# Performance work log

Measured on AMD Instinct MI355X. Metric: run time of the kernel, lower is better.

The kernel has to match this reference:

```python
import jax, jax.numpy as jnp
import numpy as np

N_NODES = 50000


def _graph_conv(x, edges, W0, b0, W1, b1):
    # Symmetric (undirected) message passing: each edge (a,b) sends x[b]->a and x[a]->b.
    src = jnp.concatenate([edges[:, 0], edges[:, 1]])  # [2E]
    dst = jnp.concatenate([edges[:, 1], edges[:, 0]])  # [2E]
    deg = jax.ops.segment_sum(jnp.ones_like(dst, dtype=x.dtype), dst, num_segments=N_NODES)
    deg = jnp.maximum(deg, 1.0)  # avoid div-by-zero for isolated nodes
    agg = jax.ops.segment_sum(x[src], dst, num_segments=N_NODES) / deg[:, None]  # [N, F]
    # self transform + normalized-neighbor transform
    return x @ W0 + b0 + agg @ W1 + b1


def setup_inputs() -> dict:
    key = jax.random.key(0)
    ks = jax.random.split(key, 10)
    feats = [256, 512, 256]  # [in] + hidden + [out]
    inp = {
        "vert_features": jax.random.normal(ks[0], (N_NODES, feats[0]), dtype=jnp.float32),
        "edges": jax.random.randint(ks[1], (400000, 2), 0, N_NODES, dtype=jnp.int64),
    }
    kidx = 2
    for l, (fi, fo) in enumerate(zip(feats[:-1], feats[1:])):
        s = 1.0 / np.sqrt(fi)
        inp[f"W0_{l}"] = jax.random.normal(ks[kidx], (fi, fo), dtype=jnp.float32) * s
        inp[f"b0_{l}"] = jnp.zeros((fo,), dtype=jnp.float32)
        inp[f"W1_{l}"] = jax.random.normal(ks[kidx + 1], (fi, fo), dtype=jnp.float32) * s
        inp[f"b1_{l}"] = jnp.zeros((fo,), dtype=jnp.float32)
        kidx += 2
    return inp


def reference(vert_features, edges, W0_0, b0_0, W1_0, b1_0, W0_1, b0_1, W1_1, b1_1):
    # layer 0 + ReLU
    x = _graph_conv(vert_features, edges, W0_0, b0_0, W1_0, b1_0)
    x = jax.nn.relu(x)
    # final layer (no activation)
    x = _graph_conv(x, edges, W0_1, b0_1, W1_1, b1_1)
    return x
```

## Files before the change

kernel.cpp:

```cpp
#include <hip/hip_runtime.h>
#include <stdint.h>

typedef __bf16  bf16x8 __attribute__((ext_vector_type(8)));
typedef float   f32x4  __attribute__((ext_vector_type(4)));
typedef unsigned short u16x8 __attribute__((ext_vector_type(8)));

__device__ __forceinline__ unsigned short f2bf(float f) {
  unsigned int u = __float_as_uint(f);
  u += 0x7fffu + ((u >> 16) & 1u);
  return (unsigned short)(u >> 16);
}
__device__ __forceinline__ float bflo(unsigned int v) { return __uint_as_float(v << 16); }
__device__ __forceinline__ float bfhi(unsigned int v) { return __uint_as_float(v & 0xffff0000u); }

__device__ __forceinline__ int edges_are_i64(const int* __restrict__ eg) {
  return (eg[1] | eg[3] | eg[5] | eg[7]) == 0;
}

__global__ void phase1_kernel(const float* __restrict__ x, unsigned short* __restrict__ A0, int n,
                              const int* __restrict__ eg, int* __restrict__ deg, int E,
                              const float* __restrict__ W00, const float* __restrict__ W10,
                              const float* __restrict__ W01, const float* __restrict__ W11,
                              const float* __restrict__ b00, const float* __restrict__ b10,
                              const float* __restrict__ b01, const float* __restrict__ b11,
                              unsigned short* __restrict__ Bt1, unsigned short* __restrict__ Bt2,
                              float* __restrict__ bias1, float* __restrict__ bias2) {
  const int i = blockIdx.x * 256 + threadIdx.x;
  if (i < n * 64) {
    const int row = i >> 6, c4 = i & 63;
    const float4 v = ((const float4*)x)[i];
    ushort4 o;
    o.x = f2bf(v.x); o.y = f2bf(v.y); o.z = f2bf(v.z); o.w = f2bf(v.w);
    *(ushort4*)&A0[(size_t)row * 512 + c4 * 4] = o;
  }
  if (i < 512 * 512) {
    const int nn = i >> 9, k = i & 511;
    const float v1 = (k < 256) ? W00[k * 512 + nn] : W10[(k - 256) * 512 + nn];
    Bt1[i] = f2bf(v1);
    const float v2 = (nn < 256) ? W01[k * 256 + nn] : W11[k * 256 + (nn - 256)];
    Bt2[i] = f2bf(v2);
    if (i < 512) {
      bias1[i] = b00[i] + b10[i];
      bias2[i] = (i < 256) ? (b01[i] + b11[i]) : 0.f;
    }
  }
  if (i < E) {
    int a, b;
    if (edges_are_i64(eg)) { a = eg[4 * i]; b = eg[4 * i + 2]; }
    else                   { a = eg[2 * i]; b = eg[2 * i + 1]; }
    if ((unsigned)a < (unsigned)n && (unsigned)b < (unsigned)n) {
      atomicAdd(&deg[a], 1);
      atomicAdd(&deg[b], 1);
    }
  }
}

__global__ void block_sum_kernel(const int* __restrict__ deg, int* __restrict__ bsum, int n) {
  const int t = threadIdx.x;
  const int i = blockIdx.x * 1024 + t;
  int v = (i < n) ? deg[i] : 0;
  #pragma unroll
  for (int d = 32; d > 0; d >>= 1) v += __shfl_xor(v, d);
  __shared__ int ws[16];
  if ((t & 63) == 0) ws[t >> 6] = v;
  __syncthreads();
  if (t < 16) {
    int s = ws[t];
    #pragma unroll
    for (int d = 1; d < 16; d <<= 1) s += __shfl_xor(s, d);
    if (t == 0) bsum[blockIdx.x] = s;
  }
}

__global__ void scan_bsum_kernel(int* __restrict__ bsum, int* __restrict__ off, int nb, int n) {
  const int l = threadIdx.x;
  int v = (l < nb) ? bsum[l] : 0;
  const int orig = v;
  #pragma unroll
  for (int d = 1; d < 64; d <<= 1) {
    int u = __shfl_up(v, d);
    if (l >= d) v += u;
  }
  if (l < nb) bsum[l] = v - orig;
  if (l == nb - 1) off[n] = v;
}

__global__ void scan_final_kernel(const int* __restrict__ deg, const int* __restrict__ bsum,
                                  int* __restrict__ off, float* __restrict__ invd,
                                  int* __restrict__ curp, int n) {
  const int t = threadIdx.x;
  const int i = blockIdx.x * 1024 + t;
  const int lane = t & 63, wid = t >> 6;
  const int v = (i < n) ? deg[i] : 0;
  int s = v;
  #pragma unroll
  for (int d = 1; d < 64; d <<= 1) {
    int u = __shfl_up(s, d);
    if (lane >= d) s += u;
  }
  __shared__ int ws[16];
  if (lane == 63) ws[wid] = s;
  __syncthreads();
  if (t < 16) {
    int w = ws[t];
    #pragma unroll
    for (int d = 1; d < 16; d <<= 1) {
      int u = __shfl_up(w, d);
      if (t >= d) w += u;
    }
    ws[t] = w;
  }
  __syncthreads();
  const int add = (wid > 0) ? ws[wid - 1] : 0;
  const int incl = s + add;
  if (i < n) {
    off[i] = bsum[blockIdx.x] + incl - v;
    invd[i] = 1.f / (float)(v > 1 ? v : 1);
    curp[i] = 0;
  }
}

__global__ void fill_kernel(const int* __restrict__ eg,
                            const int* __restrict__ off, int* __restrict__ cur,
                            int* __restrict__ adj, int E, int n) {
  const int e = blockIdx.x * 256 + threadIdx.x;
  if (e >= E) return;
  int a, b;
  if (edges_are_i64(eg)) { a = eg[4 * e]; b = eg[4 * e + 2]; }
  else                   { a = eg[2 * e]; b = eg[2 * e + 1]; }
  if ((unsigned)a >= (unsigned)n || (unsigned)b >= (unsigned)n) return;
  int p = atomicAdd(&cur[b], 1); adj[off[b] + p] = a;
  int q = atomicAdd(&cur[a], 1); adj[off[a] + q] = b;
}

template<int MODE>
__global__ __launch_bounds__(256) void agg_wide_kernel(
    const unsigned short* __restrict__ T, unsigned short* A0w, float* out,
    const int* __restrict__ adj, const int* __restrict__ off,
    const float* __restrict__ invd, int n) {
  const int node = blockIdx.x * 4 + (threadIdx.x >> 6);
  if (node >= n) return;
  const int lane = threadIdx.x & 63;
  const int half = lane >> 5;
  const int cq = lane & 31;
  constexpr size_t RS = (MODE == 0) ? 512 : 256;
  const int s = off[node], e = off[node + 1];
  float a0 = 0.f, a1 = 0.f, a2 = 0.f, a3 = 0.f, a4 = 0.f, a5 = 0.f, a6 = 0.f, a7 = 0.f;
  for (int base = s; base < e; base += 64) {
    const int cnt = min(64, e - base);
    const int idxv = (lane < cnt) ? adj[base + lane] : 0;
    for (int j = 0; j < cnt; j += 8) {
      uint4 v0 = make_uint4(0u, 0u, 0u, 0u), v1 = v0, v2 = v0, v3 = v0;
      const int s0 = j + 0 + half, s1 = j + 2 + half, s2 = j + 4 + half, s3 = j + 6 + half;
      const int r0 = __shfl(idxv, s0), r1 = __shfl(idxv, s1);
      const int r2 = __shfl(idxv, s2), r3 = __shfl(idxv, s3);
      if (s0 < cnt) v0 = *(const uint4*)&T[(size_t)r0 * RS + cq * 8];
      if (s1 < cnt) v1 = *(const uint4*)&T[(size_t)r1 * RS + cq * 8];
      if (s2 < cnt) v2 = *(const uint4*)&T[(size_t)r2 * RS + cq * 8];
      if (s3 < cnt) v3 = *(const uint4*)&T[(size_t)r3 * RS + cq * 8];
      a0 += bflo(v0.x) + bflo(v1.x) + bflo(v2.x) + bflo(v3.x);
      a1 += bfhi(v0.x) + bfhi(v1.x) + bfhi(v2.x) + bfhi(v3.x);
      a2 += bflo(v0.y) + bflo(v1.y) + bflo(v2.y) + bflo(v3.y);
      a3 += bfhi(v0.y) + bfhi(v1.y) + bfhi(v2.y) + bfhi(v3.y);
      a4 += bflo(v0.z) + bflo(v1.z) + bflo(v2.z) + bflo(v3.z);
      a5 += bfhi(v0.z) + bfhi(v1.z) + bfhi(v2.z) + bfhi(v3.z);
      a6 += bflo(v0.w) + bflo(v1.w) + bflo(v2.w) + bflo(v3.w);
      a7 += bfhi(v0.w) + bfhi(v1.w) + bfhi(v2.w) + bfhi(v3.w);
    }
  }
  a0 += __shfl_xor(a0, 32); a1 += __shfl_xor(a1, 32);
  a2 += __shfl_xor(a2, 32); a3 += __shfl_xor(a3, 32);
  a4 += __shfl_xor(a4, 32); a5 += __shfl_xor(a5, 32);
  a6 += __shfl_xor(a6, 32); a7 += __shfl_xor(a7, 32);
  if (half == 0) {
    const float sc = invd[node];
    if (MODE == 0) {
      u16x8 o;
      o[0] = f2bf(a0 * sc); o[1] = f2bf(a1 * sc); o[2] = f2bf(a2 * sc); o[3] = f2bf(a3 * sc);
      o[4] = f2bf(a4 * sc); o[5] = f2bf(a5 * sc); o[6] = f2bf(a6 * sc); o[7] = f2bf(a7 * sc);
      *(u16x8*)&A0w[(size_t)node * 512 + 256 + cq * 8] = o;
    } else {
      float* po = &out[(size_t)node * 256 + cq * 8];
      float4 p0 = *(float4*)po;
      float4 p1 = *(float4*)(po + 4);
      p0.x += sc * a0; p0.y += sc * a1; p0.z += sc * a2; p0.w += sc * a3;
      p1.x += sc * a4; p1.y += sc * a5; p1.z += sc * a6; p1.w += sc * a7;
      *(float4*)po = p0;
      *(float4*)(po + 4) = p1;
    }
  }
}

template<int MODE>
__global__ __launch_bounds__(256, 2) void gemm_kernel(
    const unsigned short* __restrict__ A, const unsigned short* __restrict__ Bt,
    const float* __restrict__ bias,
    unsigned short* __restrict__ Hout, float* __restrict__ Pout, unsigned short* __restrict__ Zout,
    int M_real, int nwg) {
  constexpr int K = 512;
  constexpr int BK = 64;
  constexpr int NT = K / BK;
  __shared__ unsigned short sm[4][128 * BK];
  const int t = threadIdx.x;
  const int lane = t & 63;
  const int wid = t >> 6;
  const int wr = wid >> 1;
  const int wc = wid & 1;

  const int orig = blockIdx.x;
  const int q = nwg >> 3, r = nwg & 7;
  const int xcd = orig & 7, bidx = orig >> 3;
  const int wgid = (xcd < r ? xcd * (q + 1) : r * (q + 1) + (xcd - r) * q) + bidx;
  const int m0 = (wgid >> 2) * 128;
  const int n0 = (wgid & 3) * 128;

  f32x4 acc[4][4];
  #pragma unroll
  for (int m = 0; m < 4; ++m)
    #pragma unroll
    for (int n = 0; n < 4; ++n)
      acc[m][n] = f32x4{0.f, 0.f, 0.f, 0.f};

  const int srow = t >> 3;
  const int schunk = t & 7;

  auto stage = [&](int buf, int kt) {
    #pragma unroll
    for (int i = 0; i < 4; ++i) {
      const int row = srow + i * 32;
      const int c = schunk ^ (row & 7);
      const unsigned short* ga = A + (size_t)(m0 + row) * K + kt * BK + c * 8;
      __builtin_amdgcn_global_load_lds(
          (const __attribute__((address_space(1))) unsigned int*)ga,
          (__attribute__((address_space(3))) unsigned int*)&sm[buf][(i * 256 + t) * 8], 16, 0, 0);
    }
    #pragma unroll
    for (int i = 0; i < 4; ++i) {
      const int row = srow + i * 32;
      const int c = schunk ^ (row & 7);
      const unsigned short* gb = Bt + (size_t)(n0 + row) * K + kt * BK + c * 8;
      __builtin_amdgcn_global_load_lds(
          (const __attribute__((address_space(1))) unsigned int*)gb,
          (__attribute__((address_space(3))) unsigned int*)&sm[2 + buf][(i * 256 + t) * 8], 16, 0, 0);
    }
    asm volatile("" ::: "memory");
    __builtin_amdgcn_sched_barrier(0);
  };

  auto compute = [&](int buf) {
    #pragma unroll
    for (int kk = 0; kk < 2; ++kk) {
      bf16x8 aF[4], bF[4];
      #pragma unroll
      for (int m = 0; m < 4; ++m) {
        const int row = wr * 64 + m * 16 + (lane & 15);
        const int sl = (kk * 4 + (lane >> 4)) ^ (row & 7);
        aF[m] = *(const bf16x8*)&sm[buf][row * BK + sl * 8];
      }
      #pragma unroll
      for (int n = 0; n < 4; ++n) {
        const int row = wc * 64 + n * 16 + (lane & 15);
        const int sl = (kk * 4 + (lane >> 4)) ^ (row & 7);
        bF[n] = *(const bf16x8*)&sm[2 + buf][row * BK + sl * 8];
      }
      #pragma unroll
      for (int m = 0; m < 4; ++m)
        #pragma unroll
        for (int n = 0; n < 4; ++n)
          acc[m][n] = __builtin_amdgcn_mfma_f32_16x16x32_bf16(aF[m], bF[n], acc[m][n], 0, 0, 0);
    }
  };

  stage(0, 0);
  #pragma unroll 1
  for (int kt = 0; kt < NT; ++kt) {
    if (kt + 1 < NT) stage((kt + 1) & 1, kt + 1);
    if (kt + 1 < NT) { asm volatile("s_waitcnt vmcnt(8)" ::: "memory"); }
    else             { asm volatile("s_waitcnt vmcnt(0)" ::: "memory"); }
    __builtin_amdgcn_sched_barrier(0);
    __builtin_amdgcn_s_barrier();
    __builtin_amdgcn_sched_barrier(0);
    compute(kt & 1);
    asm volatile("s_waitcnt lgkmcnt(0)" ::: "memory");
    __builtin_amdgcn_sched_barrier(0);
    __builtin_amdgcn_s_barrier();
    __builtin_amdgcn_sched_barrier(0);
  }
  __syncthreads();

  if (MODE == 0 || n0 >= 256) {
    unsigned short* ep = &sm[0][0];
    #pragma unroll
    for (int n = 0; n < 4; ++n) {
      const int lcol = wc * 64 + n * 16 + (lane & 15);
      const float bc = (MODE == 0) ? bias[n0 + lcol] : 0.f;
      #pragma unroll
      for (int m = 0; m < 4; ++m) {
        #pragma unroll
        for (int rr = 0; rr < 4; ++rr) {
          const int lr = wr * 64 + m * 16 + (lane >> 4) * 4 + rr;
          float y = acc[m][n][rr] + bc;
          if (MODE == 0) y = y > 0.f ? y : 0.f;
          ep[lr * 128 + (lcol ^ (((lr >> 2) & 7) << 4))] = f2bf(y);
        }
      }
    }
    __syncthreads();
    unsigned short* dst = (MODE == 0) ? Hout : Zout;
    const int ld = (MODE == 0) ? 512 : 256;
    const int cb0 = (MODE == 0) ? n0 : (n0 - 256);
    #pragma unroll
    for (int p = 0; p < 8; ++p) {
      const int tr = p * 16 + (t >> 4);
      const int cb = (t & 15) * 8;
      const uint4 v = *(const uint4*)&ep[tr * 128 + (cb ^ (((tr >> 2) & 7) << 4))];
      *(uint4*)&dst[(size_t)(m0 + tr) * ld + cb0 + cb] = v;
    }
  } else {
    float* ep = (float*)&sm[0][0];
    #pragma unroll
    for (int pp = 0; pp < 2; ++pp) {
      if (wr == pp) {
        #pragma unroll
        for (int n = 0; n < 4; ++n) {
          const int lcol = wc * 64 + n * 16 + (lane & 15);
          const float bc = bias[n0 + lcol];
          #pragma unroll
          for (int m = 0; m < 4; ++m)
            #pragma unroll
            for (int rr = 0; rr < 4; ++rr) {
              const int lr = m * 16 + (lane >> 4) * 4 + rr;
              ep[lr * 128 + (lcol ^ (((lr >> 2) & 7) << 4))] = acc[m][n][rr] + bc;
            }
        }
      }
      __syncthreads();
      const int tr = t >> 2;
      const int grow = m0 + pp * 64 + tr;
      if (grow < M_real) {
        #pragma unroll
        for (int j = 0; j < 8; ++j) {
          const int cb = (t & 3) * 32 + j * 4;
          const float4 v = *(const float4*)&ep[tr * 128 + (cb ^ (((tr >> 2) & 7) << 4))];
          *(float4*)&Pout[(size_t)grow * 256 + n0 + cb] = v;
        }
      }
      __syncthreads();
    }
  }
}

extern "C" void kernel_launch(void* const* d_in, const int* in_sizes, int n_in,
                              void* d_out, int out_size, void* d_ws, size_t ws_size,
                              hipStream_t stream) {
  const float* x   = (const float*)d_in[0];
  const int* edges = (const int*)d_in[1];
  const float* W00 = (const float*)d_in[2];
  const float* b00 = (const float*)d_in[3];
  const float* W10 = (const float*)d_in[4];
  const float* b10 = (const float*)d_in[5];
  const float* W01 = (const float*)d_in[6];
  const float* b01 = (const float*)d_in[7];
  const float* W11 = (const float*)d_in[8];
  const float* b11 = (const float*)d_in[9];
  float* out = (float*)d_out;

  const int n = in_sizes[0] / 256;
  const int E = in_sizes[1] / 2;
  const int Mpad = ((n + 127) / 128) * 128;

  char* p = (char*)d_ws;
  auto alloc = [&](size_t bytes) { char* r = p; p += (bytes + 255) & ~(size_t)255; return r; };
  unsigned short* A0   = (unsigned short*)alloc((size_t)Mpad * 512 * 2);
  unsigned short* H    = (unsigned short*)alloc((size_t)Mpad * 512 * 2);
  unsigned short* Z    = (unsigned short*)alloc((size_t)Mpad * 256 * 2);
  unsigned short* Bt1  = (unsigned short*)alloc(512 * 512 * 2);
  unsigned short* Bt2  = (unsigned short*)alloc(512 * 512 * 2);
  float* bias1 = (float*)alloc(512 * 4);
  float* bias2 = (float*)alloc(512 * 4);
  int*   deg   = (int*)alloc((size_t)n * 4);
  int*   curp  = (int*)alloc((size_t)n * 4);
  int*   off   = (int*)alloc((size_t)(n + 1) * 4);
  int*   bsum  = (int*)alloc(256 * 4);
  float* invd  = (float*)alloc((size_t)n * 4);
  int*   adj   = (int*)alloc((size_t)2 * E * 4);

  hipMemsetAsync(deg, 0, (size_t)n * 4, stream);

  const int p1_blocks = (n * 64 + 255) / 256;
  phase1_kernel<<<p1_blocks, 256, 0, stream>>>(x, A0, n, edges, deg, E,
                                               W00, W10, W01, W11, b00, b10, b01, b11,
                                               Bt1, Bt2, bias1, bias2);

  const int nb = (n + 1023) / 1024;
  block_sum_kernel<<<nb, 1024, 0, stream>>>(deg, bsum, n);
  scan_bsum_kernel<<<1, 64, 0, stream>>>(bsum, off, nb, n);
  scan_final_kernel<<<nb, 1024, 0, stream>>>(deg, bsum, off, invd, curp, n);
  fill_kernel<<<(E + 255) / 256, 256, 0, stream>>>(edges, off, curp, adj, E, n);

  agg_wide_kernel<0><<<(n + 3) / 4, 256, 0, stream>>>(A0, A0, nullptr, adj, off, invd, n);

  const int nwg = (Mpad / 128) * 4;
  gemm_kernel<0><<<nwg, 256, 0, stream>>>(A0, Bt1, bias1, H, nullptr, nullptr, n, nwg);
  gemm_kernel<1><<<nwg, 256, 0, stream>>>(H, Bt2, bias2, nullptr, out, Z, n, nwg);

  agg_wide_kernel<1><<<(n + 3) / 4, 256, 0, stream>>>(Z, nullptr, out, adj, off, invd, n);
}
```

Measured before the change: 321.1 us.

## Enlarge GEMM tile to 256x128 with 512-thread blocks and simpler barriers

The bf16 MFMA GEMM now uses 256x128 output tiles computed by 8 waves per block, where it used 128x128 tiles with 4 waves. Shared memory is split into separate A and B double buffers, row padding moves to 256, and the epilogues are adjusted to the taller tile. The aim is to load each B tile once for twice as many rows and to cut the number of workgroups. The hand-tuned vmcnt/lgkmcnt waits and sched barriers are replaced by plain __syncthreads, which may expose more of the load latency and drops the 2-blocks-per-CU occupancy hint.

After: 356.2 us. 1.11x slower.

```diff
diff --git a/kernel.cpp b/kernel.cpp
--- a/kernel.cpp
+++ b/kernel.cpp
@@ -192,7 +192,7 @@
 }
 
 template<int MODE>
-__global__ __launch_bounds__(256, 2) void gemm_kernel(
+__global__ __launch_bounds__(512, 1) void gemm_kernel(
     const unsigned short* __restrict__ A, const unsigned short* __restrict__ Bt,
     const float* __restrict__ bias,
     unsigned short* __restrict__ Hout, float* __restrict__ Pout, unsigned short* __restrict__ Zout,
@@ -200,7 +200,8 @@
   constexpr int K = 512;
   constexpr int BK = 64;
   constexpr int NT = K / BK;
-  __shared__ unsigned short sm[4][128 * BK];
+  __shared__ unsigned short sA[2][256 * BK];
+  __shared__ unsigned short sB[2][128 * BK];
   const int t = threadIdx.x;
   const int lane = t & 63;
   const int wid = t >> 6;
@@ -211,7 +212,7 @@
   const int q = nwg >> 3, r = nwg & 7;
   const int xcd = orig & 7, bidx = orig >> 3;
   const int wgid = (xcd < r ? xcd * (q + 1) : r * (q + 1) + (xcd - r) * q) + bidx;
-  const int m0 = (wgid >> 2) * 128;
+  const int m0 = (wgid >> 2) * 256;
   const int n0 = (wgid & 3) * 128;
 
   f32x4 acc[4][4];
@@ -227,24 +228,22 @@
   auto stage = [&](int buf, int kt) {
     #pragma unroll
     for (int i = 0; i < 4; ++i) {
-      const int row = srow + i * 32;
+      const int row = srow + i * 64;
       const int c = schunk ^ (row & 7);
       const unsigned short* ga = A + (size_t)(m0 + row) * K + kt * BK + c * 8;
       __builtin_amdgcn_global_load_lds(
           (const __attribute__((address_space(1))) unsigned int*)ga,
-          (__attribute__((address_space(3))) unsigned int*)&sm[buf][(i * 256 + t) * 8], 16, 0, 0);
-    }
-    #pragma unroll
-    for (int i = 0; i < 4; ++i) {
-      const int row = srow + i * 32;
+          (__attribute__((address_space(3))) unsigned int*)&sA[buf][(i * 512 + t) * 8], 16, 0, 0);
+    }
+    #pragma unroll
+    for (int i = 0; i < 2; ++i) {
+      const int row = srow + i * 64;
       const int c = schunk ^ (row & 7);
       const unsigned short* gb = Bt + (size_t)(n0 + row) * K + kt * BK + c * 8;
       __builtin_amdgcn_global_load_lds(
           (const __attribute__((address_space(1))) unsigned int*)gb,
-          (__attribute__((address_space(3))) unsigned int*)&sm[2 + buf][(i * 256 + t) * 8], 16, 0, 0);
-    }
-    asm volatile("" ::: "memory");
-    __builtin_amdgcn_sched_barrier(0);
+          (__attribute__((address_space(3))) unsigned int*)&sB[buf][(i * 512 + t) * 8], 16, 0, 0);
+    }
   };
 
   auto compute = [&](int buf) {
@@ -255,13 +254,13 @@
       for (int m = 0; m < 4; ++m) {
         const int row = wr * 64 + m * 16 + (lane & 15);
         const int sl = (kk * 4 + (lane >> 4)) ^ (row & 7);
-        aF[m] = *(const bf16x8*)&sm[buf][row * BK + sl * 8];
+        aF[m] = *(const bf16x8*)&sA[buf][row * BK + sl * 8];
       }
       #pragma unroll
       for (int n = 0; n < 4; ++n) {
         const int row = wc * 64 + n * 16 + (lane & 15);
         const int sl = (kk * 4 + (lane >> 4)) ^ (row & 7);
-        bF[n] = *(const bf16x8*)&sm[2 + buf][row * BK + sl * 8];
+        bF[n] = *(const bf16x8*)&sB[buf][row * BK + sl * 8];
       }
       #pragma unroll
       for (int m = 0; m < 4; ++m)
@@ -272,24 +271,16 @@
   };
 
   stage(0, 0);
+  __syncthreads();
   #pragma unroll 1
   for (int kt = 0; kt < NT; ++kt) {
     if (kt + 1 < NT) stage((kt + 1) & 1, kt + 1);
-    if (kt + 1 < NT) { asm volatile("s_waitcnt vmcnt(8)" ::: "memory"); }
-    else             { asm volatile("s_waitcnt vmcnt(0)" ::: "memory"); }
-    __builtin_amdgcn_sched_barrier(0);
-    __builtin_amdgcn_s_barrier();
-    __builtin_amdgcn_sched_barrier(0);
     compute(kt & 1);
-    asm volatile("s_waitcnt lgkmcnt(0)" ::: "memory");
-    __builtin_amdgcn_sched_barrier(0);
-    __builtin_amdgcn_s_barrier();
-    __builtin_amdgcn_sched_barrier(0);
-  }
-  __syncthreads();
+    __syncthreads();
+  }
 
   if (MODE == 0 || n0 >= 256) {
-    unsigned short* ep = &sm[0][0];
+    unsigned short* ep = &sA[0][0];
     #pragma unroll
     for (int n = 0; n < 4; ++n) {
       const int lcol = wc * 64 + n * 16 + (lane & 15);
@@ -311,16 +302,16 @@
     const int cb0 = (MODE == 0) ? n0 : (n0 - 256);
     #pragma unroll
     for (int p = 0; p < 8; ++p) {
-      const int tr = p * 16 + (t >> 4);
+      const int tr = p * 32 + (t >> 4);
       const int cb = (t & 15) * 8;
       const uint4 v = *(const uint4*)&ep[tr * 128 + (cb ^ (((tr >> 2) & 7) << 4))];
       *(uint4*)&dst[(size_t)(m0 + tr) * ld + cb0 + cb] = v;
     }
   } else {
-    float* ep = (float*)&sm[0][0];
+    float* ep = (float*)&sA[0][0];
     #pragma unroll
     for (int pp = 0; pp < 2; ++pp) {
-      if (wr == pp) {
+      if ((wr >> 1) == pp) {
         #pragma unroll
         for (int n = 0; n < 4; ++n) {
           const int lcol = wc * 64 + n * 16 + (lane & 15);
@@ -329,14 +320,14 @@
           for (int m = 0; m < 4; ++m)
             #pragma unroll
             for (int rr = 0; rr < 4; ++rr) {
-              const int lr = m * 16 + (lane >> 4) * 4 + rr;
+              const int lr = (wr & 1) * 64 + m * 16 + (lane >> 4) * 4 + rr;
               ep[lr * 128 + (lcol ^ (((lr >> 2) & 7) << 4))] = acc[m][n][rr] + bc;
             }
         }
       }
       __syncthreads();
       const int tr = t >> 2;
-      const int grow = m0 + pp * 64 + tr;
+      const int grow = m0 + pp * 128 + tr;
       if (grow < M_real) {
         #pragma unroll
         for (int j = 0; j < 8; ++j) {
@@ -367,7 +358,7 @@
 
   const int n = in_sizes[0] / 256;
   const int E = in_sizes[1] / 2;
-  const int Mpad = ((n + 127) / 128) * 128;
+  const int Mpad = ((n + 255) / 256) * 256;
 
   char* p = (char*)d_ws;
   auto alloc = [&](size_t bytes) { char* r = p; p += (bytes + 255) & ~(size_t)255; return r; };
@@ -400,9 +391,9 @@
 
   agg_wide_kernel<0><<<(n + 3) / 4, 256, 0, stream>>>(A0, A0, nullptr, adj, off, invd, n);
 
-  const int nwg = (Mpad / 128) * 4;
-  gemm_kernel<0><<<nwg, 256, 0, stream>>>(A0, Bt1, bias1, H, nullptr, nullptr, n, nwg);
-  gemm_kernel<1><<<nwg, 256, 0, stream>>>(H, Bt2, bias2, nullptr, out, Z, n, nwg);
+  const int nwg = (Mpad / 256) * 4;
+  gemm_kernel<0><<<nwg, 512, 0, stream>>>(A0, Bt1, bias1, H, nullptr, nullptr, n, nwg);
+  gemm_kernel<1><<<nwg, 512, 0, stream>>>(H, Bt2, bias2, nullptr, out, Z, n, nwg);
 
   agg_wide_kernel<1><<<(n + 3) / 4, 256, 0, stream>>>(Z, nullptr, out, adj, off, invd, n);
 }
```
